# Kernel tuning notes

Hardware: AMD Instinct MI355X
Metric: run time of the kernel (lower is better)

## Reference

```python
import math
import jax, jax.numpy as jnp
import numpy as np
from jax.scipy.special import erf

SIGMA = 0.5  # RegLoss sigma
N, C, D = 1048576, 10, 64


def setup_inputs() -> dict:
    key = jax.random.key(0)
    k1, k2, k3 = jax.random.split(key, 3)
    yhat = jax.random.randint(k1, (N,), 0, C)
    yg = jax.random.normal(k2, (N, C), dtype=jnp.float32)
    u_zg = jax.random.normal(k3, (N, D), dtype=jnp.float32)
    lmbd = jnp.float32(0.1)
    return {"yhat": yhat, "yg": yg, "u_zg": u_zg, "lmbd": lmbd}


def reference(yhat, yg, u_zg, lmbd):
    K = yg.shape[-1]          # classes; yhat values index this axis
    Dg = u_zg.shape[-1]
    inv = 1.0 / (SIGMA * math.sqrt(2.0))
    # elementwise erf regularizer, summed per row: f(u) = 0.5 - 0.5*erf((-1/2 - u)/(sigma*sqrt(2)))
    row_reg = jnp.sum(0.5 - 0.5 * erf((-0.5 - u_zg) * inv), axis=-1)      # [N]
    # per-row cross entropy with target = its own cluster id (unique-class loop collapses to this)
    row_ce = jax.nn.logsumexp(yg, axis=-1) - jnp.take_along_axis(yg, yhat[:, None], axis=-1)[:, 0]  # [N]
    ones = jnp.ones_like(row_ce)
    counts = jax.ops.segment_sum(ones, yhat, num_segments=K)              # [K]
    seg_reg = jax.ops.segment_sum(row_reg, yhat, num_segments=K)
    seg_ce = jax.ops.segment_sum(row_ce, yhat, num_segments=K)
    present = counts > 0
    denom = jnp.where(present, counts, 1.0)
    reg_c = seg_reg / (denom * Dg)   # mean over N_c * D elements per class
    aux_c = seg_ce / denom           # mean CE per class
    n_unique = jnp.sum(present.astype(jnp.float32))
    reg_loss = jnp.sum(jnp.where(present, reg_c, 0.0)) / n_unique
    aux_loss = jnp.sum(jnp.where(present, aux_c, 0.0)) / n_unique
    return aux_loss + lmbd * reg_loss
```

## Files before the change

kernel.cpp:

```cpp
#include <hip/hip_runtime.h>
#include <math.h>

#define N_ROWS 1048576
#define C_CLS 10
#define D_DIM 64
#define NBLK 2048
#define NTHR 256
#define NBLK_B 256
#define NBLK_A (NBLK - NBLK_B)
#define NWAVES_A (NBLK_A * (NTHR / 64))
#define NWAVES_B (NBLK_B * (NTHR / 64))

__device__ __forceinline__ float f_reg(float u) {
    float z  = fmaf(2.0f, u, 1.0f);
    float z2 = z * z;
    float a  = z * fmaf(0.1017966f, z2, 2.3048496f);
    float e  = __builtin_amdgcn_exp2f(-a);
    return __builtin_amdgcn_rcpf(1.0f + e);
}

__device__ __forceinline__ float red16(float t) {
    t += __shfl_xor(t, 1);
    t += __shfl_xor(t, 2);
    t += __shfl_xor(t, 4);
    t += __shfl_xor(t, 8);
    return t;
}

__device__ __forceinline__ int nt_load_i(const int* p) {
    return __builtin_nontemporal_load(p);
}
__device__ __forceinline__ float2 nt_load_f2(const float* p) {
    unsigned long long v = __builtin_nontemporal_load((const unsigned long long*)p);
    return __builtin_bit_cast(float2, v);
}

__global__ __launch_bounds__(256) void aux_main(
    const int* __restrict__ yhat,
    const float* __restrict__ yg,
    const float* __restrict__ u_zg,
    float* __restrict__ ws)
{
    __shared__ float s_reg[C_CLS];
    __shared__ float s_ce[C_CLS];
    __shared__ float s_cnt[C_CLS];
    __shared__ float s_yg[NTHR / 64][64 * 11];
    const int tid = threadIdx.x;
    if (tid < C_CLS) { s_reg[tid] = 0.f; s_ce[tid] = 0.f; s_cnt[tid] = 0.f; }
    __syncthreads();

    const int lane = tid & 63;
    const int wv = tid >> 6;
    const int sub = lane >> 4;

    if (blockIdx.x >= NBLK_B) {
        const int gwave = (blockIdx.x - NBLK_B) * (NTHR / 64) + wv;
        const int NG = N_ROWS / 4;
        const float4* __restrict__ u4 = (const float4*)u_zg;
        int g = gwave;
        for (; g + 3 * NWAVES_A < NG; g += 4 * NWAVES_A) {
            const int g1 = g + NWAVES_A, g2 = g + 2 * NWAVES_A, g3 = g + 3 * NWAVES_A;
            float4 v0 = u4[(size_t)g  * 64 + lane];
            float4 v1 = u4[(size_t)g1 * 64 + lane];
            float4 v2 = u4[(size_t)g2 * 64 + lane];
            float4 v3 = u4[(size_t)g3 * 64 + lane];
            int c0 = nt_load_i(&yhat[g  * 4 + sub]);
            int c1 = nt_load_i(&yhat[g1 * 4 + sub]);
            int c2 = nt_load_i(&yhat[g2 * 4 + sub]);
            int c3 = nt_load_i(&yhat[g3 * 4 + sub]);
            float t0 = f_reg(v0.x) + f_reg(v0.y) + f_reg(v0.z) + f_reg(v0.w);
            float t1 = f_reg(v1.x) + f_reg(v1.y) + f_reg(v1.z) + f_reg(v1.w);
            float t2 = f_reg(v2.x) + f_reg(v2.y) + f_reg(v2.z) + f_reg(v2.w);
            float t3 = f_reg(v3.x) + f_reg(v3.y) + f_reg(v3.z) + f_reg(v3.w);
            t0 = red16(t0); t1 = red16(t1); t2 = red16(t2); t3 = red16(t3);
            if ((lane & 15) == 0) {
                atomicAdd(&s_reg[c0], t0);
                atomicAdd(&s_reg[c1], t1);
                atomicAdd(&s_reg[c2], t2);
                atomicAdd(&s_reg[c3], t3);
            }
        }
        for (; g < NG; g += NWAVES_A) {
            float4 v = u4[(size_t)g * 64 + lane];
            int c = nt_load_i(&yhat[g * 4 + sub]);
            float t = f_reg(v.x) + f_reg(v.y) + f_reg(v.z) + f_reg(v.w);
            t = red16(t);
            if ((lane & 15) == 0) atomicAdd(&s_reg[c], t);
        }
    } else {
        const int NCHUNK = N_ROWS / 64;
        const int gwaveB = blockIdx.x * (NTHR / 64) + wv;
        float* __restrict__ myw = s_yg[wv];
        for (int chunk = gwaveB; chunk < NCHUNK; chunk += NWAVES_B) {
            const float* __restrict__ cb = yg + (size_t)chunk * 640;
#pragma unroll
            for (int k = 0; k < 5; ++k) {
                float2 r = nt_load_f2(cb + k * 128 + 2 * lane);
                int f0 = k * 128 + 2 * lane;
                int r0 = f0 / 10;
                int c0 = f0 - r0 * 10;
                myw[r0 * 11 + c0]     = r.x;
                myw[r0 * 11 + c0 + 1] = r.y;
            }
            const float* __restrict__ my = &myw[lane * 11];
            float y0 = my[0], y1 = my[1], y2 = my[2], y3 = my[3], y4 = my[4];
            float y5 = my[5], y6 = my[6], y7 = my[7], y8 = my[8], y9 = my[9];
            int row = chunk * 64 + lane;
            int c = nt_load_i(&yhat[row]);
            float m = fmaxf(fmaxf(fmaxf(y0, y1), fmaxf(y2, y3)),
                     fmaxf(fmaxf(fmaxf(y4, y5), fmaxf(y6, y7)),
                           fmaxf(y8, y9)));
            float s = __expf(y0 - m) + __expf(y1 - m)
                    + __expf(y2 - m) + __expf(y3 - m)
                    + __expf(y4 - m) + __expf(y5 - m)
                    + __expf(y6 - m) + __expf(y7 - m)
                    + __expf(y8 - m) + __expf(y9 - m);
            float ce = m + __logf(s) - my[c];
            atomicAdd(&s_ce[c], ce);
            atomicAdd(&s_cnt[c], 1.0f);
        }
    }

    __syncthreads();
    if (tid < 3 * C_CLS) {
        float v = (tid < C_CLS) ? s_reg[tid]
                : (tid < 2 * C_CLS) ? s_ce[tid - C_CLS]
                : s_cnt[tid - 2 * C_CLS];
        ws[(size_t)tid * NBLK + blockIdx.x] = v;
    }
}

__global__ __launch_bounds__(1024) void aux_final(
    const float* __restrict__ ws,
    const float* __restrict__ lmbd,
    float* __restrict__ out)
{
    __shared__ double s_tot[32];
    const int tid = threadIdx.x;
    const int lane = tid & 63;
    const int wave = tid >> 6;

    for (int e = wave; e < 3 * C_CLS; e += 16) {
        const float4* p = (const float4*)(ws + (size_t)e * NBLK);
        double acc = 0.0;
#pragma unroll
        for (int i = 0; i < 8; ++i) {
            float4 v = p[lane + 64 * i];
            acc += (double)v.x + (double)v.y + (double)v.z + (double)v.w;
        }
        for (int off = 32; off > 0; off >>= 1)
            acc += __shfl_xor(acc, off);
        if (lane == 0) s_tot[e] = acc;
    }
    __syncthreads();
    if (tid == 0) {
        double sreg = 0.0, sce = 0.0, nu = 0.0;
        for (int k = 0; k < C_CLS; ++k) {
            double cnt = s_tot[2 * C_CLS + k];
            if (cnt > 0.0) {
                sreg += s_tot[k] / (cnt * (double)D_DIM);
                sce  += s_tot[C_CLS + k] / cnt;
                nu += 1.0;
            }
        }
        out[0] = (float)(sce / nu + (double)lmbd[0] * (sreg / nu));
    }
}

extern "C" void kernel_launch(void* const* d_in, const int* in_sizes, int n_in,
                              void* d_out, int out_size, void* d_ws, size_t ws_size,
                              hipStream_t stream) {
    const int*   yhat = (const int*)d_in[0];
    const float* yg   = (const float*)d_in[1];
    const float* u_zg = (const float*)d_in[2];
    const float* lmbd = (const float*)d_in[3];
    float* out = (float*)d_out;
    float* ws  = (float*)d_ws;

    aux_main<<<NBLK, NTHR, 0, stream>>>(yhat, yg, u_zg, ws);
    aux_final<<<1, 1024, 0, stream>>>(ws, lmbd, out);
}
```

Before: 58.78 us.

## Shift tail of u_zg work onto CE blocks and drop nontemporal loads

Reserves the final 16 groups per CE wave of the u_zg regularizer work for the blocks that handle the cross-entropy rows, so those blocks pick up part of the regularizer work after their CE loop. The aim is to balance load between the two block roles so neither finishes much later than the other. It also replaces nontemporal loads with ordinary loads for yhat and yg, which changes cache behaviour. The risk is that CE blocks become the critical path if the tail share is too large.

New measurement: 61.58 us. +4.8%, slower.

```diff
diff --git a/kernel.cpp b/kernel.cpp
--- a/kernel.cpp
+++ b/kernel.cpp
@@ -10,6 +10,10 @@
 #define NBLK_A (NBLK - NBLK_B)
 #define NWAVES_A (NBLK_A * (NTHR / 64))
 #define NWAVES_B (NBLK_B * (NTHR / 64))
+#define NG (N_ROWS / 4)
+#define TAILK 4
+#define TAIL_GROUPS (4 * TAILK * NWAVES_B)
+#define GA_END (NG - TAIL_GROUPS)
 
 __device__ __forceinline__ float f_reg(float u) {
     float z  = fmaf(2.0f, u, 1.0f);
@@ -25,14 +29,6 @@
     t += __shfl_xor(t, 4);
     t += __shfl_xor(t, 8);
     return t;
-}
-
-__device__ __forceinline__ int nt_load_i(const int* p) {
-    return __builtin_nontemporal_load(p);
-}
-__device__ __forceinline__ float2 nt_load_f2(const float* p) {
-    unsigned long long v = __builtin_nontemporal_load((const unsigned long long*)p);
-    return __builtin_bit_cast(float2, v);
 }
 
 __global__ __launch_bounds__(256) void aux_main(
@@ -52,22 +48,21 @@
     const int lane = tid & 63;
     const int wv = tid >> 6;
     const int sub = lane >> 4;
+    const float4* __restrict__ u4 = (const float4*)u_zg;
 
     if (blockIdx.x >= NBLK_B) {
         const int gwave = (blockIdx.x - NBLK_B) * (NTHR / 64) + wv;
-        const int NG = N_ROWS / 4;
-        const float4* __restrict__ u4 = (const float4*)u_zg;
         int g = gwave;
-        for (; g + 3 * NWAVES_A < NG; g += 4 * NWAVES_A) {
+        for (; g + 3 * NWAVES_A < GA_END; g += 4 * NWAVES_A) {
             const int g1 = g + NWAVES_A, g2 = g + 2 * NWAVES_A, g3 = g + 3 * NWAVES_A;
             float4 v0 = u4[(size_t)g  * 64 + lane];
             float4 v1 = u4[(size_t)g1 * 64 + lane];
             float4 v2 = u4[(size_t)g2 * 64 + lane];
             float4 v3 = u4[(size_t)g3 * 64 + lane];
-            int c0 = nt_load_i(&yhat[g  * 4 + sub]);
-            int c1 = nt_load_i(&yhat[g1 * 4 + sub]);
-            int c2 = nt_load_i(&yhat[g2 * 4 + sub]);
-            int c3 = nt_load_i(&yhat[g3 * 4 + sub]);
+            int c0 = yhat[g  * 4 + sub];
+            int c1 = yhat[g1 * 4 + sub];
+            int c2 = yhat[g2 * 4 + sub];
+            int c3 = yhat[g3 * 4 + sub];
             float t0 = f_reg(v0.x) + f_reg(v0.y) + f_reg(v0.z) + f_reg(v0.w);
             float t1 = f_reg(v1.x) + f_reg(v1.y) + f_reg(v1.z) + f_reg(v1.w);
             float t2 = f_reg(v2.x) + f_reg(v2.y) + f_reg(v2.z) + f_reg(v2.w);
@@ -80,9 +75,9 @@
                 atomicAdd(&s_reg[c3], t3);
             }
         }
-        for (; g < NG; g += NWAVES_A) {
+        for (; g < GA_END; g += NWAVES_A) {
             float4 v = u4[(size_t)g * 64 + lane];
-            int c = nt_load_i(&yhat[g * 4 + sub]);
+            int c = yhat[g * 4 + sub];
             float t = f_reg(v.x) + f_reg(v.y) + f_reg(v.z) + f_reg(v.w);
             t = red16(t);
             if ((lane & 15) == 0) atomicAdd(&s_reg[c], t);
@@ -95,7 +90,7 @@
             const float* __restrict__ cb = yg + (size_t)chunk * 640;
 #pragma unroll
             for (int k = 0; k < 5; ++k) {
-                float2 r = nt_load_f2(cb + k * 128 + 2 * lane);
+                float2 r = *(const float2*)(cb + k * 128 + 2 * lane);
                 int f0 = k * 128 + 2 * lane;
                 int r0 = f0 / 10;
                 int c0 = f0 - r0 * 10;
@@ -106,7 +101,7 @@
             float y0 = my[0], y1 = my[1], y2 = my[2], y3 = my[3], y4 = my[4];
             float y5 = my[5], y6 = my[6], y7 = my[7], y8 = my[8], y9 = my[9];
             int row = chunk * 64 + lane;
-            int c = nt_load_i(&yhat[row]);
+            int c = yhat[row];
             float m = fmaxf(fmaxf(fmaxf(y0, y1), fmaxf(y2, y3)),
                      fmaxf(fmaxf(fmaxf(y4, y5), fmaxf(y6, y7)),
                            fmaxf(y8, y9)));
@@ -119,6 +114,30 @@
             atomicAdd(&s_ce[c], ce);
             atomicAdd(&s_cnt[c], 1.0f);
         }
+        int g = GA_END + gwaveB;
+#pragma unroll 1
+        for (int it = 0; it < TAILK; ++it, g += 4 * NWAVES_B) {
+            const int g1 = g + NWAVES_B, g2 = g + 2 * NWAVES_B, g3 = g + 3 * NWAVES_B;
+            float4 v0 = u4[(size_t)g  * 64 + lane];
+            float4 v1 = u4[(size_t)g1 * 64 + lane];
+            float4 v2 = u4[(size_t)g2 * 64 + lane];
+            float4 v3 = u4[(size_t)g3 * 64 + lane];
+            int c0 = yhat[g  * 4 + sub];
+            int c1 = yhat[g1 * 4 + sub];
+            int c2 = yhat[g2 * 4 + sub];
+            int c3 = yhat[g3 * 4 + sub];
+            float t0 = f_reg(v0.x) + f_reg(v0.y) + f_reg(v0.z) + f_reg(v0.w);
+            float t1 = f_reg(v1.x) + f_reg(v1.y) + f_reg(v1.z) + f_reg(v1.w);
+            float t2 = f_reg(v2.x) + f_reg(v2.y) + f_reg(v2.z) + f_reg(v2.w);
+            float t3 = f_reg(v3.x) + f_reg(v3.y) + f_reg(v3.z) + f_reg(v3.w);
+            t0 = red16(t0); t1 = red16(t1); t2 = red16(t2); t3 = red16(t3);
+            if ((lane & 15) == 0) {
+                atomicAdd(&s_reg[c0], t0);
+                atomicAdd(&s_reg[c1], t1);
+                atomicAdd(&s_reg[c2], t2);
+                atomicAdd(&s_reg[c3], t3);
+            }
+        }
     }
 
     __syncthreads();
```
